# Optimization experiments

Measured on AMD Instinct MI355X. Metric: run time of the kernel, lower is better.

## Reference

```python
import jax, jax.numpy as jnp
import numpy as np

N_NODES = 50000
IN_CH = 128
HIDDEN = 64
OUT = 32
HEADS = 4


def _gat_conv(x, src, dst, W, a_src, a_dst, b, heads, ch, concat):
    """PyG-style GATConv (eval mode, self-loops already in src/dst)."""
    N = x.shape[0]
    h = (x @ W).reshape(N, heads, ch)                      # [N,H,C]
    asrc = jnp.einsum('nhc,hc->nh', h, a_src)              # [N,H]
    adst = jnp.einsum('nhc,hc->nh', h, a_dst)              # [N,H]
    e = jax.nn.leaky_relu(asrc[src] + adst[dst], 0.2)      # [E,H]
    # segment softmax over edges grouped by destination node
    m = jax.ops.segment_max(e, dst, num_segments=N)        # [N,H]
    e = jnp.exp(e - m[dst])
    z = jax.ops.segment_sum(e, dst, num_segments=N)        # [N,H]
    alpha = e / (z[dst] + 1e-16)                           # [E,H]
    out = jax.ops.segment_sum(h[src] * alpha[:, :, None], dst, num_segments=N)  # [N,H,C]
    out = out.reshape(N, heads * ch) if concat else out.mean(axis=1)
    return out + b


def _layer_norm(x, g, b):
    mu = x.mean(axis=-1, keepdims=True)
    var = ((x - mu) ** 2).mean(axis=-1, keepdims=True)
    return (x - mu) * jax.lax.rsqrt(var + 1e-5) * g + b


def setup_inputs() -> dict:
    key = jax.random.key(0)
    ks = jax.random.split(key, 20)
    HID = HEADS * HIDDEN  # 256
    s = 0.1
    inp = {
        'x': jax.random.normal(ks[0], (N_NODES, IN_CH), jnp.float32),
        'edge_index': jax.random.randint(ks[1], (2, 800000), 0, N_NODES, jnp.int64 if jax.config.jax_enable_x64 else jnp.int32),
        # conv1
        'W1': jax.random.normal(ks[2], (IN_CH, HID), jnp.float32) * s,
        'a1_src': jax.random.normal(ks[3], (HEADS, HIDDEN), jnp.float32) * s,
        'a1_dst': jax.random.normal(ks[4], (HEADS, HIDDEN), jnp.float32) * s,
        'b1': jnp.zeros((HID,), jnp.float32),
        'g1': jnp.ones((HID,), jnp.float32),
        'be1': jnp.zeros((HID,), jnp.float32),
        # conv2
        'W2': jax.random.normal(ks[5], (HID, HID), jnp.float32) * s,
        'a2_src': jax.random.normal(ks[6], (HEADS, HIDDEN), jnp.float32) * s,
        'a2_dst': jax.random.normal(ks[7], (HEADS, HIDDEN), jnp.float32) * s,
        'b2': jnp.zeros((HID,), jnp.float32),
        'g2': jnp.ones((HID,), jnp.float32),
        'be2': jnp.zeros((HID,), jnp.float32),
        # conv3 (heads=1)
        'W3': jax.random.normal(ks[8], (HID, OUT), jnp.float32) * s,
        'a3_src': jax.random.normal(ks[9], (1, OUT), jnp.float32) * s,
        'a3_dst': jax.random.normal(ks[10], (1, OUT), jnp.float32) * s,
        'b3': jnp.zeros((OUT,), jnp.float32),
    }
    return inp


def reference(x, edge_index, W1, a1_src, a1_dst, b1, g1, be1,
              W2, a2_src, a2_dst, b2, g2, be2,
              W3, a3_src, a3_dst, b3):
    N = x.shape[0]
    loops = jnp.arange(N, dtype=edge_index.dtype)
    ei = jnp.concatenate([edge_index, jnp.stack([loops, loops])], axis=1)
    src, dst = ei[0], ei[1]
    h = _gat_conv(x, src, dst, W1, a1_src, a1_dst, b1, HEADS, HIDDEN, True)
    h = jax.nn.elu(_layer_norm(h, g1, be1))
    h = _gat_conv(h, src, dst, W2, a2_src, a2_dst, b2, HEADS, HIDDEN, True)
    h = jax.nn.elu(_layer_norm(h, g2, be2))
    return _gat_conv(h, src, dst, W3, a3_src, a3_dst, b3, 1, OUT, True)
```

## Files before the change

kernel.cpp:

```cpp
#include <hip/hip_runtime.h>
#include <math.h>

#define NN 50000

typedef __attribute__((ext_vector_type(8))) short bf16x8;
typedef __attribute__((ext_vector_type(4))) float f32x4;

__device__ inline float wred_max(float v){
  #pragma unroll
  for(int s=32;s>0;s>>=1) v=fmaxf(v,__shfl_xor(v,s,64));
  return v;
}
__device__ inline float wred_sum(float v){
  #pragma unroll
  for(int s=32;s>0;s>>=1) v+=__shfl_xor(v,s,64);
  return v;
}
__device__ inline float lrelu(float x){ return x>0.f? x : 0.2f*x; }
__device__ inline float rlf(float v,int l){ return __int_as_float(__builtin_amdgcn_readlane(__float_as_int(v),l)); }

__device__ inline ushort f2bf(float f){
  union{float f;unsigned u;} v; v.f=f;
  unsigned u=v.u;
  return (ushort)((u + 0x7fffu + ((u>>16)&1u)) >> 16);
}
__device__ inline float bflo(unsigned u){ return __uint_as_float(u<<16); }
__device__ inline float bfhi(unsigned u){ return __uint_as_float(u&0xffff0000u); }

__device__ inline void gload_lds16(const void* g, void* l){
  __builtin_amdgcn_global_load_lds((const __attribute__((address_space(1))) void*)g,
                                   (__attribute__((address_space(3))) void*)l, 16, 0, 0);
}

__global__ void casttr3_k(const float* __restrict__ W1,const float* __restrict__ W2,
                          const float* __restrict__ W3,
                          ushort* __restrict__ w1t,ushort* __restrict__ w2t,ushort* __restrict__ w3t){
  int i=blockIdx.x*256+threadIdx.x;
  if(i<32768){ int k=i>>8, n=i&255; w1t[n*128+k]=f2bf(W1[i]); }
  else if(i<98304){ int j=i-32768; int k=j>>8, n=j&255; w2t[n*256+k]=f2bf(W2[j]); }
  else { int j=i-98304; int k=j>>5, n=j&31; w3t[n*256+k]=f2bf(W3[j]); }
}

__global__ void hist_k(const int* __restrict__ dstA,int* __restrict__ counts,int E){
  int i=blockIdx.x*blockDim.x+threadIdx.x;
  if(i<E) atomicAdd(&counts[dstA[i]],1);
}

__global__ __launch_bounds__(1024) void scan1_k(int* __restrict__ counts,int* __restrict__ offs,
                                                int* __restrict__ bsum,int N){
  __shared__ int stot[16];
  int t=threadIdx.x; int lane=t&63, wv=t>>6;
  int base=blockIdx.x*1024;
  int orig=(base+t<N)?counts[base+t]:0;
  int v=orig;
  #pragma unroll
  for(int s=1;s<64;s<<=1){ int u=__shfl_up(v,s,64); if(lane>=s) v+=u; }
  if(lane==63) stot[wv]=v;
  __syncthreads();
  if(wv==0){
    int tv=(lane<16)?stot[lane]:0;
    #pragma unroll
    for(int s=1;s<16;s<<=1){ int u=__shfl_up(tv,s,64); if(lane>=s) tv+=u; }
    if(lane<16) stot[lane]=tv;
  }
  __syncthreads();
  int wpref=(wv>0)?stot[wv-1]:0;
  if(base+t<N){ offs[base+t]=wpref+v-orig; counts[base+t]=0; }
  if(t==1023) bsum[blockIdx.x]=stot[15];
}
__global__ __launch_bounds__(1024) void scan3_k(int* __restrict__ offs,const int* __restrict__ bsum,int N,int E){
  __shared__ int sbase;
  int t=threadIdx.x;
  if(t<64){
    int v=(t<(int)blockIdx.x)?bsum[t]:0;
    #pragma unroll
    for(int s=32;s>0;s>>=1) v+=__shfl_xor(v,s,64);
    if(t==0) sbase=v;
  }
  __syncthreads();
  int i=blockIdx.x*1024+t;
  if(i<N) offs[i]+=sbase;
  if(i==N-1) offs[N]=E;
}

__global__ void scatter_k(const int* __restrict__ srcA,const int* __restrict__ dstA,
                          const int* __restrict__ offs,int* cur,int* __restrict__ ssrc,int E){
  int i=blockIdx.x*blockDim.x+threadIdx.x;
  if(i<E){ int d=dstA[i]; int p=offs[d]+atomicAdd(&cur[d],1); ssrc[p]=srcA[i]; }
}

template<int WR,int WC,int MI,int NI,int DOTM,int AF32>
__global__ __launch_bounds__(256,2) void gemm_bf16_k(const void* __restrict__ Av,
    const ushort* __restrict__ Bt, ushort* __restrict__ C,
    const float* __restrict__ aS, const float* __restrict__ aD,
    float* __restrict__ as_, float* __restrict__ ad_,
    int M, int N, int K){
  constexpr int BM = WR*MI*16;
  constexpr int BN = WC*NI*16;
  __shared__ ushort sA[BM*32];
  __shared__ ushort sB[BN*32];
  int tid=threadIdx.x;
  int lane=tid&63, w=tid>>6;
  int wr=w/WC, wc=w%WC;
  int bm=blockIdx.y*BM, bn=blockIdx.x*BN;
  f32x4 acc[MI][NI]={};

  for(int k0=0;k0<K;k0+=32){
    if constexpr (AF32){
      const float* A=(const float*)Av;
      #pragma unroll
      for(int p=0;p<(BM*4)/256;p++){
        int idx=tid+p*256;
        int r=idx>>2, cs=idx&3;
        int c=cs^(r&3);
        int gr=min(bm+r,M-1);
        float4 v0=*(const float4*)(A+(size_t)gr*K+k0+c*8);
        float4 v1=*(const float4*)(A+(size_t)gr*K+k0+c*8+4);
        ulonglong2 pk;
        pk.x=(unsigned long long)f2bf(v0.x)|((unsigned long long)f2bf(v0.y)<<16)
            |((unsigned long long)f2bf(v0.z)<<32)|((unsigned long long)f2bf(v0.w)<<48);
        pk.y=(unsigned long long)f2bf(v1.x)|((unsigned long long)f2bf(v1.y)<<16)
            |((unsigned long long)f2bf(v1.z)<<32)|((unsigned long long)f2bf(v1.w)<<48);
        *(ulonglong2*)(sA+r*32+cs*8)=pk;
      }
    } else {
      const ushort* A=(const ushort*)Av;
      #pragma unroll
      for(int rr=0;rr<2;rr++){
        int rbase=w*32+rr*16;
        int r=rbase+(lane>>2);
        int cs=lane&3;
        int c=cs^(r&3);
        int gr=min(bm+r,M-1);
        gload_lds16(A+(size_t)gr*K+k0+c*8, sA+rbase*32);
      }
    }
    {
      #pragma unroll
      for(int i=0;i<(BN/16+3)/4;i++){
        int ii=w+i*4;
        if(ii<BN/16){
          int rbase=ii*16;
          int r=rbase+(lane>>2);
          int cs=lane&3;
          int c=cs^(r&3);
          gload_lds16(Bt+(size_t)(bn+r)*K+k0+c*8, sB+rbase*32);
        }
      }
    }
    __syncthreads();
    bf16x8 af[MI], bf[NI];
    #pragma unroll
    for(int m=0;m<MI;m++){
      int rA=(wr*MI+m)*16+(lane&15);
      af[m]=*(bf16x8*)(sA+rA*32+(((lane>>4)^(rA&3))*8));
    }
    #pragma unroll
    for(int n=0;n<NI;n++){
      int rB=(wc*NI+n)*16+(lane&15);
      bf[n]=*(bf16x8*)(sB+rB*32+(((lane>>4)^(rB&3))*8));
    }
    #pragma unroll
    for(int m=0;m<MI;m++)
      #pragma unroll
      for(int n=0;n<NI;n++)
        acc[m][n]=__builtin_amdgcn_mfma_f32_16x16x32_bf16(af[m],bf[n],acc[m][n],0,0,0);
    __syncthreads();
  }
  int rb=lane>>4, cl=lane&15;
  float av[NI], dv[NI];
  #pragma unroll
  for(int n=0;n<NI;n++){
    int gc=bn+(wc*NI+n)*16+cl;
    if constexpr (DOTM!=0){ av[n]=aS[gc]; dv[n]=aD[gc]; }
    else { av[n]=0.f; dv[n]=0.f; }
  }
  #pragma unroll
  for(int m=0;m<MI;m++){
    #pragma unroll
    for(int i=0;i<4;i++){
      int gr=bm+(wr*MI+m)*16+rb*4+i;
      if constexpr (DOTM==1){
        int h=(bn>>6)+wc;
        float ps=0.f,pd=0.f;
        #pragma unroll
        for(int n=0;n<NI;n++){ ps+=acc[m][n][i]*av[n]; pd+=acc[m][n][i]*dv[n]; }
        #pragma unroll
        for(int msk=1;msk<16;msk<<=1){
          ps+=__shfl_xor(ps,msk,64); pd+=__shfl_xor(pd,msk,64);
        }
        if(cl==0 && gr<M){ as_[gr*4+h]=ps; ad_[gr*4+h]=pd; }
      } else if constexpr (DOTM==2){
        float ps=0.f,pd=0.f;
        #pragma unroll
        for(int n=0;n<NI;n++){ ps+=acc[m][n][i]*av[n]; pd+=acc[m][n][i]*dv[n]; }
        #pragma unroll
        for(int msk=1;msk<16;msk<<=1){
          ps+=__shfl_xor(ps,msk,64); pd+=__shfl_xor(pd,msk,64);
        }
        if(cl==0 && gr<M){ as_[gr]=ps; ad_[gr]=pd; }
      }
      if(gr<M){
        #pragma unroll
        for(int n=0;n<NI;n++){
          int gc=bn+(wc*NI+n)*16+cl;
          int pos = (DOTM==1) ? (4*(gc&63)+(gc>>6)) : gc;
          C[(size_t)gr*N+pos]=f2bf(acc[m][n][i]);
        }
      }
    }
  }
}

__global__ __launch_bounds__(256) void agg4_k(const ushort* __restrict__ hb,
    const float* __restrict__ as_,const float* __restrict__ ad_,
    const int* __restrict__ offs,const int* __restrict__ ssrc,
    const float* __restrict__ bias,const float* __restrict__ g,const float* __restrict__ be,
    ushort* __restrict__ outb,int N){
  __shared__ float wlds[4][64][4];
  int lane=threadIdx.x&63, wv=threadIdx.x>>6;
  int n=blockIdx.x*4+wv; if(n>=N) return;
  int lane4=lane*4;
  float ad[4], es[4];
  #pragma unroll
  for(int k=0;k<4;k++) ad[k]=ad_[n*4+k];
  #pragma unroll
  for(int k=0;k<4;k++) es[k]=lrelu(as_[n*4+k]+ad[k]);
  int o0=offs[n],o1=offs[n+1];
  int cnt=o1-o0;
  float m[4], inv[4], acc[4];

  if(cnt<=64){
    int sv=0;
    float lv[4]={-1e30f,-1e30f,-1e30f,-1e30f};
    if(lane<cnt){
      sv=ssrc[o0+lane];
      float4 avv=*(const float4*)(as_+(size_t)sv*4);
      lv[0]=lrelu(avv.x+ad[0]); lv[1]=lrelu(avv.y+ad[1]);
      lv[2]=lrelu(avv.z+ad[2]); lv[3]=lrelu(avv.w+ad[3]);
    }
    #pragma unroll
    for(int k=0;k<4;k++) m[k]=fmaxf(es[k],wred_max(lv[k]));
    float w4[4];
    #pragma unroll
    for(int k=0;k<4;k++) w4[k]=(lane<cnt)?__expf(lv[k]-m[k]):0.f;
    #pragma unroll
    for(int k=0;k<4;k++){
      float z=wred_sum(w4[k])+__expf(es[k]-m[k]);
      inv[k]=1.f/(z+1e-16f);
    }
    #pragma unroll
    for(int k=0;k<4;k++) w4[k]*=inv[k];
    *(float4*)&wlds[wv][lane][0]=make_float4(w4[0],w4[1],w4[2],w4[3]);
    asm volatile("s_waitcnt lgkmcnt(0)":::"memory");
    {
      uint2 u=*(const uint2*)(hb+(size_t)n*256+lane4);
      float hv[4]={bflo(u.x),bfhi(u.x),bflo(u.y),bfhi(u.y)};
      #pragma unroll
      for(int k=0;k<4;k++) acc[k]=__expf(es[k]-m[k])*inv[k]*hv[k];
    }
    int nbat=(cnt+7)>>3;
    for(int b=0;b<nbat;b++){
      int e0=b*8;
      uint2 u[8];
      #pragma unroll
      for(int i=0;i<8;i++){
        int s=__builtin_amdgcn_readlane(sv,e0+i);
        u[i]=*(const uint2*)(hb+((size_t)s<<8)+lane4);
      }
      #pragma unroll
      for(int i=0;i<8;i++){
        const float* wp=&wlds[wv][e0+i][0];
        acc[0]+=wp[0]*bflo(u[i].x);
        acc[1]+=wp[1]*bfhi(u[i].x);
        acc[2]+=wp[2]*bflo(u[i].y);
        acc[3]+=wp[3]*bfhi(u[i].y);
      }
    }
  } else {
    #pragma unroll
    for(int k=0;k<4;k++) m[k]=es[k];
    {
      float lm[4]={-1e30f,-1e30f,-1e30f,-1e30f};
      for(int j=o0+lane;j<o1;j+=64){
        int s=ssrc[j];
        float4 avv=*(const float4*)(as_+(size_t)s*4);
        float a[4]={avv.x,avv.y,avv.z,avv.w};
        #pragma unroll
        for(int k=0;k<4;k++) lm[k]=fmaxf(lm[k],lrelu(a[k]+ad[k]));
      }
      #pragma unroll
      for(int k=0;k<4;k++) m[k]=fmaxf(m[k],wred_max(lm[k]));
    }
    {
      float lz[4]={0.f,0.f,0.f,0.f};
      for(int j=o0+lane;j<o1;j+=64){
        int s=ssrc[j];
        float4 avv=*(const float4*)(as_+(size_t)s*4);
        float a[4]={avv.x,avv.y,avv.z,avv.w};
        #pragma unroll
        for(int k=0;k<4;k++) lz[k]+=__expf(lrelu(a[k]+ad[k])-m[k]);
      }
      #pragma unroll
      for(int k=0;k<4;k++){
        float z=wred_sum(lz[k])+__expf(es[k]-m[k]);
        inv[k]=1.f/(z+1e-16f);
      }
    }
    {
      uint2 u=*(const uint2*)(hb+(size_t)n*256+lane4);
      float hv[4]={bflo(u.x),bfhi(u.x),bflo(u.y),bfhi(u.y)};
      #pragma unroll
      for(int k=0;k<4;k++) acc[k]=__expf(es[k]-m[k])*inv[k]*hv[k];
    }
    for(int base=o0;base<o1;base+=64){
      int c2=min(64,o1-base);
      int j=base+lane;
      int sv=0; float w4[4]={0.f,0.f,0.f,0.f};
      if(j<o1){
        sv=ssrc[j];
        float4 avv=*(const float4*)(as_+(size_t)sv*4);
        float a[4]={avv.x,avv.y,avv.z,avv.w};
        #pragma unroll
        for(int k=0;k<4;k++) w4[k]=__expf(lrelu(a[k]+ad[k])-m[k])*inv[k];
      }
      for(int t=0;t<c2;t++){
        int s=__builtin_amdgcn_readlane(sv,t);
        uint2 u=*(const uint2*)(hb+(size_t)s*256+lane4);
        acc[0]+=rlf(w4[0],t)*bflo(u.x);
        acc[1]+=rlf(w4[1],t)*bfhi(u.x);
        acc[2]+=rlf(w4[2],t)*bflo(u.y);
        acc[3]+=rlf(w4[3],t)*bfhi(u.y);
      }
    }
  }
  #pragma unroll
  for(int k=0;k<4;k++) acc[k]+=bias[k*64+lane];
  float tot=wred_sum(acc[0]+acc[1]+acc[2]+acc[3]);
  float mu=tot*(1.f/256.f);
  float vs=0.f;
  #pragma unroll
  for(int k=0;k<4;k++){ float d=acc[k]-mu; vs+=d*d; }
  float var=wred_sum(vs)*(1.f/256.f);
  float r=rsqrtf(var+1e-5f);
  #pragma unroll
  for(int k=0;k<4;k++){
    float v=(acc[k]-mu)*r*g[k*64+lane]+be[k*64+lane];
    float ev= v>0.f? v : expm1f(v);
    outb[(size_t)n*256+k*64+lane]=f2bf(ev);
  }
}

__global__ __launch_bounds__(256) void agg1_k(const ushort* __restrict__ hb,
    const float* __restrict__ as_,const float* __restrict__ ad_,
    const int* __restrict__ offs,const int* __restrict__ ssrc,
    const float* __restrict__ bias,float* __restrict__ out,int N){
  int lane=threadIdx.x&63, wv=threadIdx.x>>6;
  int n=blockIdx.x*4+wv; if(n>=N) return;
  float ad=ad_[n];
  float es=lrelu(as_[n]+ad);
  int o0=offs[n],o1=offs[n+1];
  int cnt=o1-o0;
  float m, inv, acc=0.f;
  int lane32=lane&31;
  int half=lane>>5;

  if(cnt<=64){
    int sv=0; float lv=-1e30f;
    if(lane<cnt){ sv=ssrc[o0+lane]; lv=lrelu(as_[sv]+ad); }
    m=fmaxf(es,wred_max(lv));
    float w1=(lane<cnt)?__expf(lv-m):0.f;
    float z=wred_sum(w1)+__expf(es-m);
    inv=1.f/(z+1e-16f);
    w1*=inv;
    if(half==0) acc=__expf(es-m)*inv*__uint_as_float(((unsigned)hb[(size_t)n*32+lane32])<<16);
    int cnt2=(cnt+1)&~1;
    for(int t=0;t<cnt2;t+=2){
      int sL=__builtin_amdgcn_readlane(sv,t);
      int sH=__builtin_amdgcn_readlane(sv,t+1);
      float wL=rlf(w1,t), wH=rlf(w1,t+1);
      int s = half? sH : sL;
      float ww = half? wH : wL;
      float hv=__uint_as_float(((unsigned)hb[(size_t)s*32+lane32])<<16);
      acc+=ww*hv;
    }
    acc+=__shfl_xor(acc,32,64);
  } else {
    m=es;
    {
      float lm=-1e30f;
      for(int j=o0+lane;j<o1;j+=64) lm=fmaxf(lm,lrelu(as_[ssrc[j]]+ad));
      m=fmaxf(m,wred_max(lm));
    }
    {
      float lz=0.f;
      for(int j=o0+lane;j<o1;j+=64) lz+=__expf(lrelu(as_[ssrc[j]]+ad)-m);
      float z=wred_sum(lz)+__expf(es-m);
      inv=1.f/(z+1e-16f);
    }
    if(lane<32) acc=__expf(es-m)*inv*__uint_as_float(((unsigned)hb[(size_t)n*32+lane])<<16);
    for(int base=o0;base<o1;base+=64){
      int c2=min(64,o1-base);
      int j=base+lane;
      int sv=0; float w1=0.f;
      if(j<o1){ sv=ssrc[j]; w1=__expf(lrelu(as_[sv]+ad)-m)*inv; }
      for(int t=0;t<c2;t++){
        int s=__builtin_amdgcn_readlane(sv,t);
        if(lane<32) acc+=rlf(w1,t)*__uint_as_float(((unsigned)hb[(size_t)s*32+lane])<<16);
      }
    }
  }
  if(lane<32) out[(size_t)n*32+lane]=acc+bias[lane];
}

extern "C" void kernel_launch(void* const* d_in,const int* in_sizes,int n_in,
                              void* d_out,int out_size,void* d_ws,size_t ws_size,
                              hipStream_t stream){
  const float* x  =(const float*)d_in[0];
  const int*   ei =(const int*)  d_in[1];
  const float* W1 =(const float*)d_in[2];
  const float* a1s=(const float*)d_in[3];
  const float* a1d=(const float*)d_in[4];
  const float* b1 =(const float*)d_in[5];
  const float* g1 =(const float*)d_in[6];
  const float* be1=(const float*)d_in[7];
  const float* W2 =(const float*)d_in[8];
  const float* a2s=(const float*)d_in[9];
  const float* a2d=(const float*)d_in[10];
  const float* b2 =(const float*)d_in[11];
  const float* g2 =(const float*)d_in[12];
  const float* be2=(const float*)d_in[13];
  const float* W3 =(const float*)d_in[14];
  const float* a3s=(const float*)d_in[15];
  const float* a3d=(const float*)d_in[16];
  const float* b3 =(const float*)d_in[17];
  float* outp=(float*)d_out;
  int N=NN;
  int E=in_sizes[1]/2;
  const int* srcA=ei;
  const int* dstA=ei+E;

  char* w=(char*)d_ws;
  ushort* hb =(ushort*)w; w+=(size_t)N*256*2;
  ushort* h3b=(ushort*)w; w+=(size_t)N*32*2;
  ushort* obb=(ushort*)w; w+=(size_t)N*256*2;
  ushort* w1t=(ushort*)w; w+=(size_t)256*128*2;
  ushort* w2t=(ushort*)w; w+=(size_t)256*256*2;
  ushort* w3t=(ushort*)w; w+=(size_t)32*256*2;
  float* asb =(float*)w; w+=(size_t)N*4*4;
  float* adb =(float*)w; w+=(size_t)N*4*4;
  int* offs=(int*)w; w+=(size_t)(N+4)*4;
  int* cur =(int*)w; w+=(size_t)N*4;
  int* ssrc=(int*)w; w+=(size_t)E*4;
  int* bsum=(int*)w; w+=(size_t)64*4;

  int NB=(N+1023)/1024;

  hipMemsetAsync(cur,0,(size_t)N*4,stream);
  hist_k<<<(E+255)/256,256,0,stream>>>(dstA,cur,E);
  scan1_k<<<NB,1024,0,stream>>>(cur,offs,bsum,N);
  scan3_k<<<NB,1024,0,stream>>>(offs,bsum,N,E);
  scatter_k<<<(E+255)/256,256,0,stream>>>(srcA,dstA,offs,cur,ssrc,E);

  casttr3_k<<<416,256,0,stream>>>(W1,W2,W3,w1t,w2t,w3t);

  int nblkN=(N+3)/4;
  int gY128=(N+127)/128;

  gemm_bf16_k<2,2,4,4,1,1><<<dim3(2,gY128),256,0,stream>>>(x,w1t,hb,a1s,a1d,asb,adb,N,256,128);
  agg4_k<<<nblkN,256,0,stream>>>(hb,asb,adb,offs,ssrc,b1,g1,be1,obb,N);

  gemm_bf16_k<2,2,4,4,1,0><<<dim3(2,gY128),256,0,stream>>>(obb,w2t,hb,a2s,a2d,asb,adb,N,256,256);
  agg4_k<<<nblkN,256,0,stream>>>(hb,asb,adb,offs,ssrc,b2,g2,be2,obb,N);

  gemm_bf16_k<4,1,2,2,2,0><<<dim3(1,gY128),256,0,stream>>>(obb,w3t,h3b,a3s,a3d,asb,adb,N,32,256);
  agg1_k<<<nblkN,256,0,stream>>>(h3b,asb,adb,offs,ssrc,b3,outp,N);
}
```

Before: 335.7 us.

## Use natural head-major feature layout in 4-head aggregation, widen gather batches

The GEMM epilogue now stores features in natural column order instead of interleaving heads, so each lane in the aggregation kernel owns four contiguous channels of a single head. The aggregation then uses one attention weight per lane (one LDS read per edge instead of four), loads bias/gamma/beta as float4, and writes the output as one packed 64-bit store. The gather batch grows from 8 to 16 edges for more memory-level parallelism, and launch bounds request 6 blocks per CU. The larger batch raises register pressure and wastes more loads for low-degree nodes.

Result: faster. 327.4 us (-2.5%).

```diff
diff --git a/kernel.cpp b/kernel.cpp
--- a/kernel.cpp
+++ b/kernel.cpp
@@ -204,15 +204,14 @@
         #pragma unroll
         for(int n=0;n<NI;n++){
           int gc=bn+(wc*NI+n)*16+cl;
-          int pos = (DOTM==1) ? (4*(gc&63)+(gc>>6)) : gc;
-          C[(size_t)gr*N+pos]=f2bf(acc[m][n][i]);
+          C[(size_t)gr*N+gc]=f2bf(acc[m][n][i]);
         }
       }
     }
   }
 }
 
-__global__ __launch_bounds__(256) void agg4_k(const ushort* __restrict__ hb,
+__global__ __launch_bounds__(256,6) void agg4_k(const ushort* __restrict__ hb,
     const float* __restrict__ as_,const float* __restrict__ ad_,
     const int* __restrict__ offs,const int* __restrict__ ssrc,
     const float* __restrict__ bias,const float* __restrict__ g,const float* __restrict__ be,
@@ -221,6 +220,7 @@
   int lane=threadIdx.x&63, wv=threadIdx.x>>6;
   int n=blockIdx.x*4+wv; if(n>=N) return;
   int lane4=lane*4;
+  int h=lane>>4;
   float ad[4], es[4];
   #pragma unroll
   for(int k=0;k<4;k++) ad[k]=ad_[n*4+k];
@@ -254,27 +254,27 @@
     *(float4*)&wlds[wv][lane][0]=make_float4(w4[0],w4[1],w4[2],w4[3]);
     asm volatile("s_waitcnt lgkmcnt(0)":::"memory");
     {
+      float wself=__expf(es[h]-m[h])*inv[h];
       uint2 u=*(const uint2*)(hb+(size_t)n*256+lane4);
-      float hv[4]={bflo(u.x),bfhi(u.x),bflo(u.y),bfhi(u.y)};
-      #pragma unroll
-      for(int k=0;k<4;k++) acc[k]=__expf(es[k]-m[k])*inv[k]*hv[k];
-    }
-    int nbat=(cnt+7)>>3;
+      acc[0]=wself*bflo(u.x); acc[1]=wself*bfhi(u.x);
+      acc[2]=wself*bflo(u.y); acc[3]=wself*bfhi(u.y);
+    }
+    int nbat=(cnt+15)>>4;
     for(int b=0;b<nbat;b++){
-      int e0=b*8;
-      uint2 u[8];
-      #pragma unroll
-      for(int i=0;i<8;i++){
+      int e0=b*16;
+      uint2 u[16];
+      #pragma unroll
+      for(int i=0;i<16;i++){
         int s=__builtin_amdgcn_readlane(sv,e0+i);
         u[i]=*(const uint2*)(hb+((size_t)s<<8)+lane4);
       }
       #pragma unroll
-      for(int i=0;i<8;i++){
-        const float* wp=&wlds[wv][e0+i][0];
-        acc[0]+=wp[0]*bflo(u[i].x);
-        acc[1]+=wp[1]*bfhi(u[i].x);
-        acc[2]+=wp[2]*bflo(u[i].y);
-        acc[3]+=wp[3]*bfhi(u[i].y);
+      for(int i=0;i<16;i++){
+        float we=wlds[wv][e0+i][h];
+        acc[0]+=we*bflo(u[i].x);
+        acc[1]+=we*bfhi(u[i].x);
+        acc[2]+=we*bflo(u[i].y);
+        acc[3]+=we*bfhi(u[i].y);
       }
     }
   } else {
@@ -308,10 +308,10 @@
       }
     }
     {
+      float wself=__expf(es[h]-m[h])*inv[h];
       uint2 u=*(const uint2*)(hb+(size_t)n*256+lane4);
-      float hv[4]={bflo(u.x),bfhi(u.x),bflo(u.y),bfhi(u.y)};
-      #pragma unroll
-      for(int k=0;k<4;k++) acc[k]=__expf(es[k]-m[k])*inv[k]*hv[k];
+      acc[0]=wself*bflo(u.x); acc[1]=wself*bfhi(u.x);
+      acc[2]=wself*bflo(u.y); acc[3]=wself*bfhi(u.y);
     }
     for(int base=o0;base<o1;base+=64){
       int c2=min(64,o1-base);
@@ -326,16 +326,20 @@
       }
       for(int t=0;t<c2;t++){
         int s=__builtin_amdgcn_readlane(sv,t);
+        float wa=rlf(w4[0],t),wb=rlf(w4[1],t),wc=rlf(w4[2],t),wd=rlf(w4[3],t);
+        float we = h<2 ? (h==0?wa:wb) : (h==2?wc:wd);
         uint2 u=*(const uint2*)(hb+(size_t)s*256+lane4);
-        acc[0]+=rlf(w4[0],t)*bflo(u.x);
-        acc[1]+=rlf(w4[1],t)*bfhi(u.x);
-        acc[2]+=rlf(w4[2],t)*bflo(u.y);
-        acc[3]+=rlf(w4[3],t)*bfhi(u.y);
-      }
-    }
-  }
-  #pragma unroll
-  for(int k=0;k<4;k++) acc[k]+=bias[k*64+lane];
+        acc[0]+=we*bflo(u.x);
+        acc[1]+=we*bfhi(u.x);
+        acc[2]+=we*bflo(u.y);
+        acc[3]+=we*bfhi(u.y);
+      }
+    }
+  }
+  {
+    float4 bv=*(const float4*)(bias+lane4);
+    acc[0]+=bv.x; acc[1]+=bv.y; acc[2]+=bv.z; acc[3]+=bv.w;
+  }
   float tot=wred_sum(acc[0]+acc[1]+acc[2]+acc[3]);
   float mu=tot*(1.f/256.f);
   float vs=0.f;
@@ -343,12 +347,18 @@
   for(int k=0;k<4;k++){ float d=acc[k]-mu; vs+=d*d; }
   float var=wred_sum(vs)*(1.f/256.f);
   float r=rsqrtf(var+1e-5f);
+  float4 gv=*(const float4*)(g+lane4);
+  float4 bev=*(const float4*)(be+lane4);
+  float gg[4]={gv.x,gv.y,gv.z,gv.w};
+  float bb[4]={bev.x,bev.y,bev.z,bev.w};
+  unsigned long long pk=0;
   #pragma unroll
   for(int k=0;k<4;k++){
-    float v=(acc[k]-mu)*r*g[k*64+lane]+be[k*64+lane];
+    float v=(acc[k]-mu)*r*gg[k]+bb[k];
     float ev= v>0.f? v : expm1f(v);
-    outb[(size_t)n*256+k*64+lane]=f2bf(ev);
-  }
+    pk|=((unsigned long long)f2bf(ev))<<(16*k);
+  }
+  *(unsigned long long*)(outb+(size_t)n*256+lane4)=pk;
 }
 
 __global__ __launch_bounds__(256) void agg1_k(const ushort* __restrict__ hb,
```
